# Kernel optimization log

Measured on AMD Instinct MI355X. Metric: run time of the kernel, lower is better.

The kernel has to match this reference:

```python
import jax, jax.numpy as jnp
import numpy as np

M = 7            # window size
N = M * M        # tokens per window = 49
HEADS = 8
DIM = 256
NW = 64          # windows per image (56x56 feature map / 7x7 windows)
B_WIN = 4096     # B * num_windows (batch 64 images)


def _relative_position_index():
    # Standard Swin relative position index, shape (N, N), values in [0, (2M-1)^2)
    coords = np.stack(np.meshgrid(np.arange(M), np.arange(M), indexing='ij'))  # (2,M,M)
    coords = coords.reshape(2, -1)                                             # (2,N)
    rel = coords[:, :, None] - coords[:, None, :]                              # (2,N,N)
    rel = rel.transpose(1, 2, 0).astype(np.int32)                              # (N,N,2)
    rel[..., 0] += M - 1
    rel[..., 1] += M - 1
    rel[..., 0] *= 2 * M - 1
    return rel.sum(-1)  # (N,N)


def setup_inputs() -> dict:
    key = jax.random.key(0)
    ks = jax.random.split(key, 7)
    x = jax.random.normal(ks[0], (B_WIN, N, DIM), dtype=jnp.float32)
    # Shifted-window attention mask: 0 where attend, -100 where blocked
    mask = jnp.where(jax.random.uniform(ks[1], (NW, N, N)) > 0.5, 0.0, -100.0).astype(jnp.float32)
    rel_index = jnp.asarray(_relative_position_index(), dtype=jnp.int32)
    qkv_w = jax.random.normal(ks[2], (3 * DIM, DIM), dtype=jnp.float32) * 0.02
    qkv_b = jax.random.normal(ks[3], (3 * DIM,), dtype=jnp.float32) * 0.02
    proj_w = jax.random.normal(ks[4], (DIM, DIM), dtype=jnp.float32) * 0.02
    proj_b = jax.random.normal(ks[5], (DIM,), dtype=jnp.float32) * 0.02
    bias_table = jax.random.normal(ks[6], ((2 * M - 1) ** 2, HEADS), dtype=jnp.float32) * 0.02
    return {"x": x, "mask": mask, "rel_index": rel_index, "qkv_w": qkv_w,
            "qkv_b": qkv_b, "proj_w": proj_w, "proj_b": proj_b, "bias_table": bias_table}


def reference(x, mask, rel_index, qkv_w, qkv_b, proj_w, proj_b, bias_table):
    B, n, C = x.shape                      # (B*nW, 49, 256)
    h = bias_table.shape[1]
    d = C // h
    scale = d ** -0.5
    # qkv projection -> (3, B, h, n, d)
    qkv = (x @ qkv_w.T + qkv_b).reshape(B, n, 3, h, d).transpose(2, 0, 3, 1, 4)
    q, k, v = qkv[0] * scale, qkv[1], qkv[2]
    attn = jnp.einsum('bhnd,bhmd->bhnm', q, k)              # (B,h,n,n)
    # relative position bias gather: (n,n) index into (169,h) -> (h,n,n)
    bias = bias_table[rel_index].transpose(2, 0, 1)
    attn = attn + bias[None]
    # per-window mask: attn viewed as (B//nW, nW, h, n, n) + mask (nW,1,n,n)
    nW = mask.shape[0]
    attn = attn.reshape(B // nW, nW, h, n, n) + mask[None, :, None]
    attn = jax.nn.softmax(attn.reshape(B, h, n, n), axis=-1)
    out = jnp.einsum('bhnm,bhmd->bhnd', attn, v)            # (B,h,n,d)
    out = out.transpose(0, 2, 1, 3).reshape(B, n, C)
    return out @ proj_w.T + proj_b
```

## Files before the change

### kernel.cpp

```cpp
#include <hip/hip_runtime.h>
#include <cstdint>


typedef __attribute__((ext_vector_type(8))) short short8;
typedef __attribute__((ext_vector_type(4))) float floatx4;

__device__ __forceinline__ ushort f2bf(float f) {
    uint32_t u = __float_as_uint(f);
    u += 0x7FFFu + ((u >> 16) & 1u);
    return (ushort)(u >> 16);
}

__device__ __forceinline__ uint32_t cvtpk(float lo, float hi) {
    uint32_t r;
    asm("v_cvt_pk_bf16_f32 %0, %1, %2" : "=v"(r) : "v"(lo), "v"(hi));
    return r;
}

__global__ __launch_bounds__(256) void k_cvt_w(const float* __restrict__ qw,
                                               const float* __restrict__ pw,
                                               ushort* __restrict__ qwb,
                                               ushort* __restrict__ pwb) {
    int i = blockIdx.x * 256 + threadIdx.x;
    if (i < 196608) qwb[i] = f2bf(qw[i]);
    else            pwb[i - 196608] = f2bf(pw[i - 196608]);
}

__global__ __launch_bounds__(256) void k_comb(const float* __restrict__ mask,
                                              const int* __restrict__ rel,
                                              const float* __restrict__ bt,
                                              float* __restrict__ comb) {
    const int wh = blockIdx.x;
    const int w = wh >> 3, h = wh & 7;
    const float* mw = mask + (size_t)w * 2401;
    float* out = comb + (size_t)wh * 4096;
    for (int e = threadIdx.x; e < 49 * 64; e += 256) {
        const int n = e >> 6, m = e & 63;
        out[e] = (m < 49) ? mw[n * 49 + m] + bt[rel[n * 49 + m] * 8 + h] : 0.0f;
    }
}

__global__ __launch_bounds__(512, 2) void k_mono(
        const ushort* __restrict__ qwb, const float* __restrict__ x,
        const float* __restrict__ qb, const float* __restrict__ comb,
        const ushort* __restrict__ pwb, const float* __restrict__ pb,
        float* __restrict__ out) {
    __shared__ ushort smem[68608];
    ushort* xb    = smem;
    ushort* q_lds = smem + 16384;
    ushort* k_lds = smem + 33280;
    ushort* vt    = smem + 50176;

    const int t = threadIdx.x;
    const int w = t >> 6, l = t & 63;
    const int g = l >> 4, li = l & 15;
    const int blk = blockIdx.x;
    const int wdw = blk & 63;

    {
        const int n = t >> 3, seg = t & 7;
        if (n < 49) {
            const float* src = x + ((size_t)blk * 49 + n) * 256 + seg * 32;
#pragma unroll
            for (int c4 = 0; c4 < 4; ++c4) {
                const float4 a  = *(const float4*)(src + c4 * 8);
                const float4 b2 = *(const float4*)(src + c4 * 8 + 4);
                uint4 u;
                u.x = cvtpk(a.x, a.y);  u.y = cvtpk(a.z, a.w);
                u.z = cvtpk(b2.x, b2.y); u.w = cvtpk(b2.z, b2.w);
                const int j = seg * 4 + c4;
                *(uint4*)(xb + n * 256 + ((j ^ (n & 7)) * 8)) = u;
            }
        } else {
            const uint4 z = {0u, 0u, 0u, 0u};
#pragma unroll
            for (int c4 = 0; c4 < 4; ++c4) {
                const int j = seg * 4 + c4;
                *(uint4*)(xb + n * 256 + ((j ^ (n & 7)) * 8)) = z;
            }
        }
    }
    __syncthreads();

    const floatx4 zf = {0.f, 0.f, 0.f, 0.f};
    const float scale = 0.17677669529663687f;

    {
        floatx4 acc[6][4];
#pragma unroll
        for (int i = 0; i < 6; ++i)
#pragma unroll
            for (int j = 0; j < 4; ++j) acc[i][j] = zf;

#pragma unroll
        for (int kt = 0; kt < 8; ++kt) {
            short8 af[6], bfr[4];
#pragma unroll
            for (int ct = 0; ct < 6; ++ct)
                af[ct] = *(const short8*)(qwb +
                    (size_t)(w * 96 + ct * 16 + li) * 256 + kt * 32 + g * 8);
#pragma unroll
            for (int nt = 0; nt < 4; ++nt)
                bfr[nt] = *(const short8*)(xb + (nt * 16 + li) * 256 +
                    (((kt * 4 + g) ^ (li & 7)) * 8));
#pragma unroll
            for (int ct = 0; ct < 6; ++ct)
#pragma unroll
                for (int nt = 0; nt < 4; ++nt)
                    acc[ct][nt] = __builtin_amdgcn_mfma_f32_16x16x32_bf16(
                        af[ct], bfr[nt], acc[ct][nt], 0, 0, 0);
        }

#pragma unroll
        for (int ct = 0; ct < 6; ++ct) {
            const int cb = w * 96 + ct * 16 + g * 4;
            const int which = cb >> 8, head = (cb >> 5) & 7, dd0 = cb & 31;
            const float4 b4 = *(const float4*)(qb + cb);
#pragma unroll
            for (int nt = 0; nt < 4; ++nt) {
                const int n = nt * 16 + li;
                const float v0 = acc[ct][nt][0] + b4.x;
                const float v1 = acc[ct][nt][1] + b4.y;
                const float v2 = acc[ct][nt][2] + b4.z;
                const float v3 = acc[ct][nt][3] + b4.w;
                if (which < 2) {
                    ushort* dst = (which == 0) ? q_lds : k_lds;
                    uint2 pk2;
                    pk2.x = cvtpk(v0, v1);
                    pk2.y = cvtpk(v2, v3);
                    *(uint2*)(dst + n * 264 + head * 32 + dd0) = pk2;
                } else {
                    const int rb = head * 32 + dd0;
                    vt[(rb + 0) * 72 + n] = f2bf(v0);
                    vt[(rb + 1) * 72 + n] = f2bf(v1);
                    vt[(rb + 2) * 72 + n] = f2bf(v2);
                    vt[(rb + 3) * 72 + n] = f2bf(v3);
                }
            }
        }
    }
    __syncthreads();

    ushort* P  = smem + w * 4608;
    ushort* ao = smem;

    short8 qf[4], kf[4], vf[2][2];
#pragma unroll
    for (int mt = 0; mt < 4; ++mt) {
        qf[mt] = *(const short8*)(q_lds + (mt * 16 + li) * 264 + w * 32 + g * 8);
        kf[mt] = *(const short8*)(k_lds + (mt * 16 + li) * 264 + w * 32 + g * 8);
    }
#pragma unroll
    for (int ks = 0; ks < 2; ++ks)
#pragma unroll
        for (int nt = 0; nt < 2; ++nt)
            vf[ks][nt] = *(const short8*)(vt + (w * 32 + nt * 16 + li) * 72 +
                                          ks * 32 + g * 8);
    __syncthreads();

    floatx4 sac[4][4];
#pragma unroll
    for (int bq = 0; bq < 4; ++bq)
#pragma unroll
        for (int ak = 0; ak < 4; ++ak)
            sac[bq][ak] = __builtin_amdgcn_mfma_f32_16x16x32_bf16(
                kf[ak], qf[bq], zf, 0, 0, 0);

    const float* cw = comb + (size_t)(wdw * 8 + w) * 4096;

#pragma unroll
    for (int bq = 0; bq < 4; ++bq) {
        const int n = bq * 16 + li;
        const float* cr = cw + n * 64 + g * 4;
        const float4 c0 = *(const float4*)(cr);
        const float4 c1 = *(const float4*)(cr + 16);
        const float4 c2 = *(const float4*)(cr + 32);
        const float c3x = cr[48];
        float v[12];
        v[0]  = sac[bq][0][0] * scale + c0.x;
        v[1]  = sac[bq][0][1] * scale + c0.y;
        v[2]  = sac[bq][0][2] * scale + c0.z;
        v[3]  = sac[bq][0][3] * scale + c0.w;
        v[4]  = sac[bq][1][0] * scale + c1.x;
        v[5]  = sac[bq][1][1] * scale + c1.y;
        v[6]  = sac[bq][1][2] * scale + c1.z;
        v[7]  = sac[bq][1][3] * scale + c1.w;
        v[8]  = sac[bq][2][0] * scale + c2.x;
        v[9]  = sac[bq][2][1] * scale + c2.y;
        v[10] = sac[bq][2][2] * scale + c2.z;
        v[11] = sac[bq][2][3] * scale + c2.w;
        const float v48 = (g == 0) ? sac[bq][3][0] * scale + c3x : -3.0e38f;
        float mx = fmaxf(fmaxf(fmaxf(v[0], v[1]), fmaxf(v[2], v[3])),
                         fmaxf(fmaxf(v[4], v[5]), fmaxf(v[6], v[7])));
        mx = fmaxf(mx, fmaxf(fmaxf(v[8], v[9]), fmaxf(v[10], v[11])));
        mx = fmaxf(mx, v48);
        mx = fmaxf(mx, __shfl_xor(mx, 16, 64));
        mx = fmaxf(mx, __shfl_xor(mx, 32, 64));
        float e[12], s = 0.f;
#pragma unroll
        for (int i = 0; i < 12; ++i) { e[i] = __expf(v[i] - mx); s += e[i]; }
        const float e48 = __expf(v48 - mx);
        s += e48;
        s += __shfl_xor(s, 16, 64);
        s += __shfl_xor(s, 32, 64);
        const float inv = 1.0f / s;
        uint2 pk;
#pragma unroll
        for (int a = 0; a < 3; ++a) {
            pk.x = cvtpk(e[a * 4 + 0] * inv, e[a * 4 + 1] * inv);
            pk.y = cvtpk(e[a * 4 + 2] * inv, e[a * 4 + 3] * inv);
            *(uint2*)(P + n * 72 + a * 16 + g * 4) = pk;
        }
        pk.x = cvtpk(e48 * inv, 0.f);
        pk.y = 0u;
        *(uint2*)(P + n * 72 + 48 + g * 4) = pk;
    }

    floatx4 oac[4][2];
#pragma unroll
    for (int mt = 0; mt < 4; ++mt)
#pragma unroll
        for (int nt = 0; nt < 2; ++nt) oac[mt][nt] = zf;
#pragma unroll
    for (int ks = 0; ks < 2; ++ks)
#pragma unroll
        for (int mt = 0; mt < 4; ++mt) {
            const short8 pf = *(const short8*)(P + (mt * 16 + li) * 72 +
                                               ks * 32 + g * 8);
            oac[mt][0] = __builtin_amdgcn_mfma_f32_16x16x32_bf16(
                pf, vf[ks][0], oac[mt][0], 0, 0, 0);
            oac[mt][1] = __builtin_amdgcn_mfma_f32_16x16x32_bf16(
                pf, vf[ks][1], oac[mt][1], 0, 0, 0);
        }

    __syncthreads();

#pragma unroll
    for (int mt = 0; mt < 4; ++mt)
#pragma unroll
        for (int rr = 0; rr < 4; ++rr) {
            const int n = mt * 16 + g * 4 + rr;
            if (n < 49) {
#pragma unroll
                for (int nt = 0; nt < 2; ++nt)
                    ao[n * 264 + w * 32 + nt * 16 + li] = f2bf(oac[mt][nt][rr]);
            }
        }
    for (int idx = l; idx < 240; idx += 64) {
        const int n = 49 + (idx >> 4);
        const int du = idx & 15;
        *(uint32_t*)(ao + n * 264 + w * 32 + du * 2) = 0u;
    }
    __syncthreads();

    floatx4 pacc[4][2];
#pragma unroll
    for (int mt = 0; mt < 4; ++mt)
#pragma unroll
        for (int nt = 0; nt < 2; ++nt) pacc[mt][nt] = zf;
#pragma unroll
    for (int kt = 0; kt < 8; ++kt) {
        short8 afr[4], wfr[2];
#pragma unroll
        for (int mt = 0; mt < 4; ++mt)
            afr[mt] = *(const short8*)(ao + (mt * 16 + li) * 264 + kt * 32 + g * 8);
#pragma unroll
        for (int nt = 0; nt < 2; ++nt)
            wfr[nt] = *(const short8*)(pwb +
                (size_t)(w * 32 + nt * 16 + li) * 256 + kt * 32 + g * 8);
#pragma unroll
        for (int mt = 0; mt < 4; ++mt)
#pragma unroll
            for (int nt = 0; nt < 2; ++nt)
                pacc[mt][nt] = __builtin_amdgcn_mfma_f32_16x16x32_bf16(
                    afr[mt], wfr[nt], pacc[mt][nt], 0, 0, 0);
    }

    float* og = out + (size_t)blk * 49 * 256;
#pragma unroll
    for (int nt = 0; nt < 2; ++nt) {
        const int c = w * 32 + nt * 16 + li;
        const float bias = pb[c];
#pragma unroll
        for (int mt = 0; mt < 4; ++mt)
#pragma unroll
            for (int r = 0; r < 4; ++r) {
                const int n = mt * 16 + g * 4 + r;
                if (n < 49) og[(size_t)n * 256 + c] = pacc[mt][nt][r] + bias;
            }
    }
}

extern "C" void kernel_launch(void* const* d_in, const int* in_sizes, int n_in,
                              void* d_out, int out_size, void* d_ws, size_t ws_size,
                              hipStream_t stream) {
    const float* x      = (const float*)d_in[0];
    const float* mask   = (const float*)d_in[1];
    const int*   rel    = (const int*)d_in[2];
    const float* qkv_w  = (const float*)d_in[3];
    const float* qkv_b  = (const float*)d_in[4];
    const float* proj_w = (const float*)d_in[5];
    const float* proj_b = (const float*)d_in[6];
    const float* bt     = (const float*)d_in[7];
    float* out = (float*)d_out;

    char* ws = (char*)d_ws;
    ushort* qwb  = (ushort*)(ws);
    ushort* pwb  = (ushort*)(ws + 393216);
    float*  comb = (float*) (ws + 524288);
    (void)ws_size; (void)in_sizes; (void)n_in; (void)out_size;

    k_cvt_w<<<dim3(1024), dim3(256), 0, stream>>>(qkv_w, proj_w, qwb, pwb);
    k_comb <<<dim3(512),  dim3(256), 0, stream>>>(mask, rel, bt, comb);
    k_mono <<<dim3(4096), dim3(512), 0, stream>>>(qwb, x, qkv_b, comb, pwb,
                                                  proj_b, out);
}
```

Before: 442.9 us.

## Assign each wave its own head's QKV rows to shrink shared memory

The QKV projection is repartitioned so each wave computes the Q, K and V columns for its own head instead of an arbitrary 96-column slice. The wave can then stage its head's Q/K/V through a small private LDS scratch region, with no block-wide exchange buffers and one fewer __syncthreads. Shared memory drops from about 137KB to about 78KB per block, which may allow more resident blocks, at the cost of extra per-wave LDS round trips for Q and K reloads.

Measured after the change: 411.5 us. 7.1% less time.

```diff
diff --git a/kernel.cpp b/kernel.cpp
--- a/kernel.cpp
+++ b/kernel.cpp
@@ -45,17 +45,19 @@
         const float* __restrict__ qb, const float* __restrict__ comb,
         const ushort* __restrict__ pwb, const float* __restrict__ pb,
         float* __restrict__ out) {
-    __shared__ ushort smem[68608];
-    ushort* xb    = smem;
-    ushort* q_lds = smem + 16384;
-    ushort* k_lds = smem + 33280;
-    ushort* vt    = smem + 50176;
+    __shared__ ushort smem[38912];
+    ushort* xb = smem;
 
     const int t = threadIdx.x;
     const int w = t >> 6, l = t & 63;
     const int g = l >> 4, li = l & 15;
     const int blk = blockIdx.x;
     const int wdw = blk & 63;
+
+    ushort* scr = smem + w * 4864;
+    ushort* vtw = smem + w * 4864 + 2560;
+    ushort* P   = smem + w * 4864;
+    ushort* ao  = smem;
 
     {
         const int n = t >> 3, seg = t & 7;
@@ -85,78 +87,90 @@
     const floatx4 zf = {0.f, 0.f, 0.f, 0.f};
     const float scale = 0.17677669529663687f;
 
-    {
-        floatx4 acc[6][4];
-#pragma unroll
-        for (int i = 0; i < 6; ++i)
-#pragma unroll
-            for (int j = 0; j < 4; ++j) acc[i][j] = zf;
-
-#pragma unroll
-        for (int kt = 0; kt < 8; ++kt) {
-            short8 af[6], bfr[4];
-#pragma unroll
-            for (int ct = 0; ct < 6; ++ct)
-                af[ct] = *(const short8*)(qwb +
-                    (size_t)(w * 96 + ct * 16 + li) * 256 + kt * 32 + g * 8);
+    const int rowbase[6] = {w * 32,       w * 32 + 16,
+                            256 + w * 32, 256 + w * 32 + 16,
+                            512 + w * 32, 512 + w * 32 + 16};
+    floatx4 acc[6][4];
+#pragma unroll
+    for (int i = 0; i < 6; ++i)
+#pragma unroll
+        for (int j = 0; j < 4; ++j) acc[i][j] = zf;
+
+#pragma unroll
+    for (int kt = 0; kt < 8; ++kt) {
+        short8 af[6], bfr[4];
+#pragma unroll
+        for (int ct = 0; ct < 6; ++ct)
+            af[ct] = *(const short8*)(qwb +
+                (size_t)(rowbase[ct] + li) * 256 + kt * 32 + g * 8);
+#pragma unroll
+        for (int nt = 0; nt < 4; ++nt)
+            bfr[nt] = *(const short8*)(xb + (nt * 16 + li) * 256 +
+                (((kt * 4 + g) ^ (li & 7)) * 8));
+#pragma unroll
+        for (int ct = 0; ct < 6; ++ct)
 #pragma unroll
             for (int nt = 0; nt < 4; ++nt)
-                bfr[nt] = *(const short8*)(xb + (nt * 16 + li) * 256 +
-                    (((kt * 4 + g) ^ (li & 7)) * 8));
-#pragma unroll
-            for (int ct = 0; ct < 6; ++ct)
-#pragma unroll
-                for (int nt = 0; nt < 4; ++nt)
-                    acc[ct][nt] = __builtin_amdgcn_mfma_f32_16x16x32_bf16(
-                        af[ct], bfr[nt], acc[ct][nt], 0, 0, 0);
-        }
-
-#pragma unroll
-        for (int ct = 0; ct < 6; ++ct) {
-            const int cb = w * 96 + ct * 16 + g * 4;
-            const int which = cb >> 8, head = (cb >> 5) & 7, dd0 = cb & 31;
-            const float4 b4 = *(const float4*)(qb + cb);
-#pragma unroll
-            for (int nt = 0; nt < 4; ++nt) {
-                const int n = nt * 16 + li;
-                const float v0 = acc[ct][nt][0] + b4.x;
-                const float v1 = acc[ct][nt][1] + b4.y;
-                const float v2 = acc[ct][nt][2] + b4.z;
-                const float v3 = acc[ct][nt][3] + b4.w;
-                if (which < 2) {
-                    ushort* dst = (which == 0) ? q_lds : k_lds;
-                    uint2 pk2;
-                    pk2.x = cvtpk(v0, v1);
-                    pk2.y = cvtpk(v2, v3);
-                    *(uint2*)(dst + n * 264 + head * 32 + dd0) = pk2;
-                } else {
-                    const int rb = head * 32 + dd0;
-                    vt[(rb + 0) * 72 + n] = f2bf(v0);
-                    vt[(rb + 1) * 72 + n] = f2bf(v1);
-                    vt[(rb + 2) * 72 + n] = f2bf(v2);
-                    vt[(rb + 3) * 72 + n] = f2bf(v3);
-                }
-            }
-        }
+                acc[ct][nt] = __builtin_amdgcn_mfma_f32_16x16x32_bf16(
+                    af[ct], bfr[nt], acc[ct][nt], 0, 0, 0);
     }
     __syncthreads();
 
-    ushort* P  = smem + w * 4608;
-    ushort* ao = smem;
-
     short8 qf[4], kf[4], vf[2][2];
-#pragma unroll
-    for (int mt = 0; mt < 4; ++mt) {
-        qf[mt] = *(const short8*)(q_lds + (mt * 16 + li) * 264 + w * 32 + g * 8);
-        kf[mt] = *(const short8*)(k_lds + (mt * 16 + li) * 264 + w * 32 + g * 8);
+
+#pragma unroll
+    for (int ct = 0; ct < 2; ++ct) {
+        const int dd0 = ct * 16 + g * 4;
+        const float4 b4 = *(const float4*)(qb + w * 32 + dd0);
+#pragma unroll
+        for (int nt = 0; nt < 4; ++nt) {
+            const int n = nt * 16 + li;
+            uint2 pk2;
+            pk2.x = cvtpk(acc[ct][nt][0] + b4.x, acc[ct][nt][1] + b4.y);
+            pk2.y = cvtpk(acc[ct][nt][2] + b4.z, acc[ct][nt][3] + b4.w);
+            *(uint2*)(scr + n * 40 + dd0) = pk2;
+        }
+    }
+#pragma unroll
+    for (int mt = 0; mt < 4; ++mt)
+        qf[mt] = *(const short8*)(scr + (mt * 16 + li) * 40 + g * 8);
+
+#pragma unroll
+    for (int ct = 2; ct < 4; ++ct) {
+        const int dd0 = (ct - 2) * 16 + g * 4;
+        const float4 b4 = *(const float4*)(qb + 256 + w * 32 + dd0);
+#pragma unroll
+        for (int nt = 0; nt < 4; ++nt) {
+            const int n = nt * 16 + li;
+            uint2 pk2;
+            pk2.x = cvtpk(acc[ct][nt][0] + b4.x, acc[ct][nt][1] + b4.y);
+            pk2.y = cvtpk(acc[ct][nt][2] + b4.z, acc[ct][nt][3] + b4.w);
+            *(uint2*)(scr + n * 40 + dd0) = pk2;
+        }
+    }
+#pragma unroll
+    for (int mt = 0; mt < 4; ++mt)
+        kf[mt] = *(const short8*)(scr + (mt * 16 + li) * 40 + g * 8);
+
+#pragma unroll
+    for (int ct = 4; ct < 6; ++ct) {
+        const int dd0 = (ct - 4) * 16 + g * 4;
+        const float4 b4 = *(const float4*)(qb + 512 + w * 32 + dd0);
+#pragma unroll
+        for (int nt = 0; nt < 4; ++nt) {
+            const int n = nt * 16 + li;
+            vtw[(dd0 + 0) * 72 + n] = f2bf(acc[ct][nt][0] + b4.x);
+            vtw[(dd0 + 1) * 72 + n] = f2bf(acc[ct][nt][1] + b4.y);
+            vtw[(dd0 + 2) * 72 + n] = f2bf(acc[ct][nt][2] + b4.z);
+            vtw[(dd0 + 3) * 72 + n] = f2bf(acc[ct][nt][3] + b4.w);
+        }
     }
 #pragma unroll
     for (int ks = 0; ks < 2; ++ks)
 #pragma unroll
         for (int nt = 0; nt < 2; ++nt)
-            vf[ks][nt] = *(const short8*)(vt + (w * 32 + nt * 16 + li) * 72 +
+            vf[ks][nt] = *(const short8*)(vtw + (nt * 16 + li) * 72 +
                                           ks * 32 + g * 8);
-    __syncthreads();
 
     floatx4 sac[4][4];
 #pragma unroll
```
